# Performance work log

Measured on AMD Instinct MI355X. Metric: run time of the kernel, lower is better.

Reference implementation:

```python
import jax, jax.numpy as jnp
import numpy as np

H, W = 512, 512
B, C = 16, 3
PCT = 3.0  # normalization_percentile_threshold


def _make_filter_map(h, w, d0_ratio=0.05, bn=1):
    d0 = int(max(d0_ratio * min(h, w) // 2, 1))  # = 12 for 512x512
    i = np.arange(h, dtype=np.float64)[:, None]
    j = np.arange(w, dtype=np.float64)[None, :]
    d = np.full((h, w), np.inf)
    for cx, cy in ((0, 0), (0, w - 1), (h - 1, w - 1), (h - 1, 0)):
        d = np.minimum(d, np.sqrt((i - cx) ** 2 + (j - cy) ** 2))
    fm = 1.0 / (1.0 + (d0 / (d + 1.0)) ** (2 * bn))
    # torch code assigns filter_map[j, i] -> transpose (no-op for square sizes)
    return jnp.asarray(fm.T.astype(np.float32))


def setup_inputs() -> dict:
    key = jax.random.key(0)
    k1, k2 = jax.random.split(key)
    x = jax.random.normal(k1, (B, C, H, W), dtype=jnp.float32)
    mask = (jax.random.uniform(k2, (B, C, H, W)) > 0.2).astype(jnp.float32)
    filter_map = _make_filter_map(H, W)
    return {"x": x, "mask": mask, "filter_map": filter_map}


def reference(x, mask, filter_map):
    b, c, h, w = x.shape
    n = h * w
    # median_padding: torch.median returns the lower middle element -> sorted index (n-1)//2
    med = jnp.sort(x.reshape(b, c, n), axis=-1)[..., (n - 1) // 2] + 0.2  # (B,C)
    xp = mask * x + (1.0 - mask) * med[:, :, None, None]
    # Butterworth high-pass in Fourier domain
    hfc = jnp.abs(jnp.fft.ifft2(jnp.fft.fft2(xp) * filter_map)).astype(jnp.float32)
    # per-(n,c) percentile normalization; .int() truncates toward zero -> jnp.trunc
    temp = jnp.trunc(hfc * 256.0) / 256.0
    lo = jnp.percentile(temp, PCT, axis=(-2, -1), keepdims=True)
    hi = jnp.percentile(temp, 100.0 - PCT, axis=(-2, -1), keepdims=True)
    res = (hfc - lo) / (hi - lo)
    return res * mask
```

## Files before the change

kernel.cpp:

```cpp
#include <hip/hip_runtime.h>
#include <math.h>


#define HN 512
#define WN 512
#define NPIX (HN * WN)
#define NCH 48
#define MED_K 131071u
#define TWOPI 6.283185307179586f

typedef unsigned int u32;

__device__ __constant__ u32 PRANKS[4] = {7864u, 7865u, 254278u, 254279u};

__device__ __forceinline__ int rev8_9(int i) { return ((i & 7) << 6) | (i & 56) | (i >> 6); }

#define LPAD 576
__device__ __forceinline__ int padi(int i) { return i + (i >> 3); }

__device__ __forceinline__ u32 f2key(float f) {
  u32 u = __float_as_uint(f);
  return u ^ ((u & 0x80000000u) ? 0xFFFFFFFFu : 0x80000000u);
}
__device__ __forceinline__ float key2f(u32 k) {
  u32 u = (k & 0x80000000u) ? (k ^ 0x80000000u) : ~k;
  return __uint_as_float(u);
}

__device__ __forceinline__ float2 cadd(float2 a, float2 b) { return make_float2(a.x + b.x, a.y + b.y); }
__device__ __forceinline__ float2 csub(float2 a, float2 b) { return make_float2(a.x - b.x, a.y - b.y); }
__device__ __forceinline__ float2 cmul(float2 a, float2 b) {
  return make_float2(a.x * b.x - a.y * b.y, a.x * b.y + a.y * b.x);
}

template <bool INV>
__device__ __forceinline__ void dft8(float2* r) {
  const float S2 = 0.70710678118654752f;
  float2 e0, e1, e2, e3, o0, o1, o2, o3;
  {
    float2 t0 = cadd(r[0], r[4]), t1 = csub(r[0], r[4]);
    float2 t2 = cadd(r[2], r[6]), t3 = csub(r[2], r[6]);
    e0 = cadd(t0, t2); e2 = csub(t0, t2);
    if (!INV) { e1 = make_float2(t1.x + t3.y, t1.y - t3.x); e3 = make_float2(t1.x - t3.y, t1.y + t3.x); }
    else      { e1 = make_float2(t1.x - t3.y, t1.y + t3.x); e3 = make_float2(t1.x + t3.y, t1.y - t3.x); }
  }
  {
    float2 t0 = cadd(r[1], r[5]), t1 = csub(r[1], r[5]);
    float2 t2 = cadd(r[3], r[7]), t3 = csub(r[3], r[7]);
    o0 = cadd(t0, t2); o2 = csub(t0, t2);
    if (!INV) { o1 = make_float2(t1.x + t3.y, t1.y - t3.x); o3 = make_float2(t1.x - t3.y, t1.y + t3.x); }
    else      { o1 = make_float2(t1.x - t3.y, t1.y + t3.x); o3 = make_float2(t1.x + t3.y, t1.y - t3.x); }
  }
  float2 w1o, w2o, w3o;
  if (!INV) {
    w1o = make_float2(S2 * (o1.x + o1.y), S2 * (o1.y - o1.x));
    w2o = make_float2(o2.y, -o2.x);
    w3o = make_float2(S2 * (o3.y - o3.x), -S2 * (o3.x + o3.y));
  } else {
    w1o = make_float2(S2 * (o1.x - o1.y), S2 * (o1.x + o1.y));
    w2o = make_float2(-o2.y, o2.x);
    w3o = make_float2(-S2 * (o3.x + o3.y), S2 * (o3.x - o3.y));
  }
  r[0] = cadd(e0, o0); r[4] = csub(e0, o0);
  r[1] = cadd(e1, w1o); r[5] = csub(e1, w1o);
  r[2] = cadd(e2, w2o); r[6] = csub(e2, w2o);
  r[3] = cadd(e3, w3o); r[7] = csub(e3, w3o);
}

__device__ __forceinline__ void twid(float2* r, float ang) {
  float sn, cs;
  __sincosf(ang, &sn, &cs);
  float2 w = make_float2(cs, sn);
  float2 wj = w;
  r[1] = cmul(r[1], wj);
  #pragma unroll
  for (int j = 2; j < 8; ++j) { wj = cmul(wj, w); r[j] = cmul(r[j], wj); }
}

__device__ void scan_find(const u32* __restrict__ h, int per, u32 rank,
                          u32* out_bin, u32* out_pref) {
  __shared__ u32 csum[256], cpre[256];
  int t = threadIdx.x;
  u32 s = 0;
  for (int i = 0; i < per; ++i) s += h[t * per + i];
  csum[t] = s;
  __syncthreads();
  if (t == 0) { u32 a = 0; for (int i = 0; i < 256; ++i) { cpre[i] = a; a += csum[i]; } }
  __syncthreads();
  if (cpre[t] <= rank && rank < cpre[t] + csum[t]) {
    u32 acc = cpre[t];
    for (int i = 0; i < per; ++i) {
      u32 c = h[t * per + i];
      if (rank < acc + c) { *out_bin = (u32)(t * per + i); *out_pref = acc; break; }
      acc += c;
    }
  }
  __syncthreads();
}


__global__ __launch_bounds__(256) void kmed1(const float4* __restrict__ x4, u32* __restrict__ h1) {
  int ch = blockIdx.x >> 4, s = blockIdx.x & 15;
  __shared__ u32 lh[4096];
  for (int i = threadIdx.x; i < 4096; i += 256) lh[i] = 0;
  __syncthreads();
  const float4* p = x4 + (size_t)ch * (NPIX / 4) + (size_t)s * (NPIX / 64);
  for (int i = threadIdx.x; i < NPIX / 64; i += 256) {
    float4 v = p[i];
    atomicAdd(&lh[f2key(v.x) >> 20], 1u);
    atomicAdd(&lh[f2key(v.y) >> 20], 1u);
    atomicAdd(&lh[f2key(v.z) >> 20], 1u);
    atomicAdd(&lh[f2key(v.w) >> 20], 1u);
  }
  __syncthreads();
  u32* h = h1 + (size_t)ch * 4096;
  for (int i = threadIdx.x; i < 4096; i += 256) { u32 c = lh[i]; if (c) atomicAdd(&h[i], c); }
}

__global__ __launch_bounds__(256) void kscan1(const u32* __restrict__ h1, u32* sel1, u32* pref1) {
  __shared__ u32 b, p;
  scan_find(h1 + (size_t)blockIdx.x * 4096, 16, MED_K, &b, &p);
  if (threadIdx.x == 0) { sel1[blockIdx.x] = b; pref1[blockIdx.x] = p; }
}

__global__ __launch_bounds__(256) void kmed2(const float4* __restrict__ x4, u32* __restrict__ h2,
                                             const u32* __restrict__ sel1) {
  int ch = blockIdx.x >> 4, s = blockIdx.x & 15;
  u32 sh = sel1[ch];
  __shared__ u32 lh[4096];
  for (int i = threadIdx.x; i < 4096; i += 256) lh[i] = 0;
  __syncthreads();
  const float4* p = x4 + (size_t)ch * (NPIX / 4) + (size_t)s * (NPIX / 64);
  for (int i = threadIdx.x; i < NPIX / 64; i += 256) {
    float4 v = p[i];
    u32 k;
    k = f2key(v.x); if ((k >> 20) == sh) atomicAdd(&lh[(k >> 8) & 0xFFFu], 1u);
    k = f2key(v.y); if ((k >> 20) == sh) atomicAdd(&lh[(k >> 8) & 0xFFFu], 1u);
    k = f2key(v.z); if ((k >> 20) == sh) atomicAdd(&lh[(k >> 8) & 0xFFFu], 1u);
    k = f2key(v.w); if ((k >> 20) == sh) atomicAdd(&lh[(k >> 8) & 0xFFFu], 1u);
  }
  __syncthreads();
  u32* h = h2 + (size_t)ch * 4096;
  for (int i = threadIdx.x; i < 4096; i += 256) { u32 c = lh[i]; if (c) atomicAdd(&h[i], c); }
}

__global__ __launch_bounds__(256) void kscan2(const u32* __restrict__ h2, const u32* __restrict__ pref1,
                                              u32* sel2, u32* pref2) {
  __shared__ u32 b, p;
  scan_find(h2 + (size_t)blockIdx.x * 4096, 16, MED_K - pref1[blockIdx.x], &b, &p);
  if (threadIdx.x == 0) { sel2[blockIdx.x] = b; pref2[blockIdx.x] = p; }
}

__global__ __launch_bounds__(256) void kmed3(const float4* __restrict__ x4, u32* __restrict__ h3,
                                             const u32* __restrict__ sel1, const u32* __restrict__ sel2) {
  int ch = blockIdx.x >> 4, s = blockIdx.x & 15;
  u32 pre = (sel1[ch] << 12) | sel2[ch];
  __shared__ u32 lh[256];
  lh[threadIdx.x] = 0;
  __syncthreads();
  const float4* p = x4 + (size_t)ch * (NPIX / 4) + (size_t)s * (NPIX / 64);
  for (int i = threadIdx.x; i < NPIX / 64; i += 256) {
    float4 v = p[i];
    u32 k;
    k = f2key(v.x); if ((k >> 8) == pre) atomicAdd(&lh[k & 0xFFu], 1u);
    k = f2key(v.y); if ((k >> 8) == pre) atomicAdd(&lh[k & 0xFFu], 1u);
    k = f2key(v.z); if ((k >> 8) == pre) atomicAdd(&lh[k & 0xFFu], 1u);
    k = f2key(v.w); if ((k >> 8) == pre) atomicAdd(&lh[k & 0xFFu], 1u);
  }
  __syncthreads();
  u32 c = lh[threadIdx.x];
  if (c) atomicAdd(&h3[(size_t)ch * 256 + threadIdx.x], c);
}

__global__ __launch_bounds__(256) void kscan3(const u32* __restrict__ h3, const u32* __restrict__ sel1,
                                              const u32* __restrict__ sel2, const u32* __restrict__ pref1,
                                              const u32* __restrict__ pref2, float* med) {
  int ch = blockIdx.x;
  __shared__ u32 b, p;
  scan_find(h3 + (size_t)ch * 256, 1, MED_K - pref1[ch] - pref2[ch], &b, &p);
  if (threadIdx.x == 0) {
    u32 key = (sel1[ch] << 20) | (sel2[ch] << 8) | b;
    med[ch] = key2f(key) + 0.2f;
  }
}


__global__ __launch_bounds__(256) void kperm(const float* __restrict__ fmap, float* __restrict__ fmp) {
  int c = blockIdx.x;
  for (int e = threadIdx.x; e < HN; e += 256)
    fmp[(size_t)c * HN + e] = fmap[(size_t)rev8_9(e) * WN + rev8_9(c)] * (1.0f / (float)NPIX);
}


__global__ __launch_bounds__(256) void krow_fwd(const float* __restrict__ x, const float* __restrict__ mask,
                                                const float* __restrict__ med, float2* __restrict__ cbuf, int ch0) {
  int lch = blockIdx.x >> 7, rb = blockIdx.x & 127;
  int gch = ch0 + lch;
  int lane = threadIdx.x & 63, r = threadIdx.x >> 6;
  int row = rb * 4 + r;
  __shared__ float2 lds[4][LPAD];
  float2* L = lds[r];
  float mv = med[gch];
  const float* xr = x + (size_t)gch * NPIX + (size_t)row * WN;
  const float* mr = mask + (size_t)gch * NPIX + (size_t)row * WN;
  float2 rg[8];
  #pragma unroll
  for (int m = 0; m < 8; ++m) {
    float xv = xr[lane + 64 * m], mm = mr[lane + 64 * m];
    rg[m] = make_float2(mm * xv + (1.0f - mm) * mv, 0.0f);
  }
  dft8<false>(rg);
  twid(rg, (float)lane * (-TWOPI / 512.0f));
  int pb = lane + (lane >> 3);
  #pragma unroll
  for (int j = 0; j < 8; ++j) L[pb + 72 * j] = rg[j];
  __syncthreads();
  int n0 = lane & 7;
  int pb2 = 72 * (lane >> 3) + n0;
  #pragma unroll
  for (int m = 0; m < 8; ++m) rg[m] = L[pb2 + 9 * m];
  dft8<false>(rg);
  twid(rg, (float)n0 * (-TWOPI / 64.0f));
  #pragma unroll
  for (int j = 0; j < 8; ++j) L[pb2 + 9 * j] = rg[j];
  __syncthreads();
  int pc = 9 * lane;
  #pragma unroll
  for (int m = 0; m < 8; ++m) rg[m] = L[pc + m];
  dft8<false>(rg);
  #pragma unroll
  for (int j = 0; j < 8; ++j) L[pc + j] = rg[j];
  __syncthreads();
  float2* cb = cbuf + (size_t)lch * NPIX + (size_t)row * WN;
  #pragma unroll
  for (int q = 0; q < 4; ++q) {
    int e = 2 * (lane + 64 * q);
    int pe = padi(e);
    float2 a = L[pe], b = L[pe + 1];
    *(float4*)(cb + e) = make_float4(a.x, a.y, b.x, b.y);
  }
}


__global__ __launch_bounds__(512) void kcol(float2* __restrict__ cbuf, const float* __restrict__ fmp) {
  int lch = blockIdx.x >> 6;
  int c0 = (blockIdx.x & 63) << 3;
  int tid = threadIdx.x;
  int lane = tid & 63, cc = tid >> 6;
  __shared__ float2 lds[8][LPAD];
  float2* L = lds[cc];
  size_t base = (size_t)lch * NPIX + c0;
  #pragma unroll
  for (int it = 0; it < 4; ++it) {
    int g = it * 512 + tid;
    int h = g >> 2, qq = g & 3;
    float4 v = *(const float4*)(cbuf + base + (size_t)h * WN + 2 * qq);
    int ph = padi(h);
    lds[2 * qq][ph]     = make_float2(v.x, v.y);
    lds[2 * qq + 1][ph] = make_float2(v.z, v.w);
  }
  __syncthreads();
  float2 rg[8];
  int pb = lane + (lane >> 3);
  int n0 = lane & 7;
  int pb2 = 72 * (lane >> 3) + n0;
  int pc = 9 * lane;
  #pragma unroll
  for (int m = 0; m < 8; ++m) rg[m] = L[pb + 72 * m];
  dft8<false>(rg);
  twid(rg, (float)lane * (-TWOPI / 512.0f));
  #pragma unroll
  for (int j = 0; j < 8; ++j) L[pb + 72 * j] = rg[j];
  __syncthreads();
  #pragma unroll
  for (int m = 0; m < 8; ++m) rg[m] = L[pb2 + 9 * m];
  dft8<false>(rg);
  twid(rg, (float)n0 * (-TWOPI / 64.0f));
  #pragma unroll
  for (int j = 0; j < 8; ++j) L[pb2 + 9 * j] = rg[j];
  __syncthreads();
  #pragma unroll
  for (int m = 0; m < 8; ++m) rg[m] = L[pc + m];
  dft8<false>(rg);
  {
    const float* fp = fmp + (size_t)(c0 + cc) * HN + 8 * lane;
    float4 f0 = *(const float4*)fp, f1 = *(const float4*)(fp + 4);
    rg[0].x *= f0.x; rg[0].y *= f0.x;  rg[1].x *= f0.y; rg[1].y *= f0.y;
    rg[2].x *= f0.z; rg[2].y *= f0.z;  rg[3].x *= f0.w; rg[3].y *= f0.w;
    rg[4].x *= f1.x; rg[4].y *= f1.x;  rg[5].x *= f1.y; rg[5].y *= f1.y;
    rg[6].x *= f1.z; rg[6].y *= f1.z;  rg[7].x *= f1.w; rg[7].y *= f1.w;
  }
  dft8<true>(rg);
  #pragma unroll
  for (int j = 0; j < 8; ++j) L[pc + j] = rg[j];
  __syncthreads();
  #pragma unroll
  for (int m = 0; m < 8; ++m) rg[m] = L[pb2 + 9 * m];
  twid(rg, (float)n0 * (TWOPI / 64.0f));
  dft8<true>(rg);
  #pragma unroll
  for (int j = 0; j < 8; ++j) L[pb2 + 9 * j] = rg[j];
  __syncthreads();
  #pragma unroll
  for (int m = 0; m < 8; ++m) rg[m] = L[pb + 72 * m];
  twid(rg, (float)lane * (TWOPI / 512.0f));
  dft8<true>(rg);
  #pragma unroll
  for (int j = 0; j < 8; ++j) L[pb + 72 * j] = rg[j];
  __syncthreads();
  #pragma unroll
  for (int it = 0; it < 4; ++it) {
    int g = it * 512 + tid;
    int h = g >> 2, qq = g & 3;
    int ph = padi(h);
    float2 a = lds[2 * qq][ph], b = lds[2 * qq + 1][ph];
    *(float4*)(cbuf + base + (size_t)h * WN + 2 * qq) = make_float4(a.x, a.y, b.x, b.y);
  }
}


__global__ __launch_bounds__(256) void krow_inv(const float2* __restrict__ cbuf, float* __restrict__ out,
                                                u32* __restrict__ hc, int ch0) {
  int lch = blockIdx.x >> 7, rb = blockIdx.x & 127;
  int gch = ch0 + lch;
  int lane = threadIdx.x & 63, r = threadIdx.x >> 6;
  int row = rb * 4 + r;
  __shared__ float2 lds[4][LPAD];
  __shared__ u32 lh[256];
  float2* L = lds[r];
  lh[threadIdx.x] = 0;
  const float2* cb = cbuf + (size_t)lch * NPIX + (size_t)row * WN;
  #pragma unroll
  for (int q = 0; q < 4; ++q) {
    int e = 2 * (lane + 64 * q);
    float4 v = *(const float4*)(cb + e);
    int pe = padi(e);
    L[pe]     = make_float2(v.x, v.y);
    L[pe + 1] = make_float2(v.z, v.w);
  }
  __syncthreads();
  float2 rg[8];
  int pc = 9 * lane;
  #pragma unroll
  for (int m = 0; m < 8; ++m) rg[m] = L[pc + m];
  dft8<true>(rg);
  #pragma unroll
  for (int j = 0; j < 8; ++j) L[pc + j] = rg[j];
  __syncthreads();
  int n0 = lane & 7;
  int pb2 = 72 * (lane >> 3) + n0;
  #pragma unroll
  for (int m = 0; m < 8; ++m) rg[m] = L[pb2 + 9 * m];
  twid(rg, (float)n0 * (TWOPI / 64.0f));
  dft8<true>(rg);
  #pragma unroll
  for (int j = 0; j < 8; ++j) L[pb2 + 9 * j] = rg[j];
  __syncthreads();
  int pb = lane + (lane >> 3);
  #pragma unroll
  for (int m = 0; m < 8; ++m) rg[m] = L[pb + 72 * m];
  twid(rg, (float)lane * (TWOPI / 512.0f));
  dft8<true>(rg);
  float* orow = out + (size_t)gch * NPIX + (size_t)row * WN;
  #pragma unroll
  for (int j = 0; j < 8; ++j) {
    float mg = sqrtf(rg[j].x * rg[j].x + rg[j].y * rg[j].y);
    orow[lane + 64 * j] = mg;
    u32 bin = (u32)fminf(mg * 256.0f, 65535.0f);
    atomicAdd(&lh[bin >> 8], 1u);
  }
  __syncthreads();
  u32 c = lh[threadIdx.x];
  if (c) atomicAdd(&hc[(size_t)gch * 256 + threadIdx.x], c);
}


__global__ __launch_bounds__(256) void kpcts1(const u32* __restrict__ hc, u32* selc, u32* prefc) {
  int ch = blockIdx.x;
  __shared__ u32 b, p;
  for (int q = 0; q < 4; ++q) {
    scan_find(hc + (size_t)ch * 256, 1, PRANKS[q], &b, &p);
    if (threadIdx.x == 0) { selc[ch * 4 + q] = b; prefc[ch * 4 + q] = p; }
    __syncthreads();
  }
}

__global__ __launch_bounds__(256) void kpctf(const float4* __restrict__ out4, u32* __restrict__ hf,
                                             const u32* __restrict__ selc) {
  int ch = blockIdx.x >> 3, s = blockIdx.x & 7;
  u32 t0 = selc[ch * 4 + 0], t1 = selc[ch * 4 + 1], t2 = selc[ch * 4 + 2], t3 = selc[ch * 4 + 3];
  __shared__ u32 lh[1024];
  for (int i = threadIdx.x; i < 1024; i += 256) lh[i] = 0;
  __syncthreads();
  const float4* p = out4 + (size_t)ch * (NPIX / 4) + (size_t)s * (NPIX / 32);
  for (int i = threadIdx.x; i < NPIX / 32; i += 256) {
    float4 v = p[i];
    float vv[4] = {v.x, v.y, v.z, v.w};
    #pragma unroll
    for (int j = 0; j < 4; ++j) {
      u32 bin = (u32)fminf(vv[j] * 256.0f, 65535.0f);
      u32 cb = bin >> 8, fb = bin & 255u;
      if (cb == t0) atomicAdd(&lh[0 * 256 + fb], 1u);
      if (cb == t1) atomicAdd(&lh[1 * 256 + fb], 1u);
      if (cb == t2) atomicAdd(&lh[2 * 256 + fb], 1u);
      if (cb == t3) atomicAdd(&lh[3 * 256 + fb], 1u);
    }
  }
  __syncthreads();
  for (int i = threadIdx.x; i < 1024; i += 256) {
    u32 c = lh[i];
    if (c) atomicAdd(&hf[(size_t)ch * 1024 + i], c);
  }
}

__global__ __launch_bounds__(256) void kpcts2(const u32* __restrict__ hf, const u32* __restrict__ selc,
                                              const u32* __restrict__ prefc, float* lov, float* invv) {
  int ch = blockIdx.x;
  __shared__ u32 b, p;
  __shared__ u32 bins[4];
  for (int q = 0; q < 4; ++q) {
    scan_find(hf + (size_t)ch * 1024 + q * 256, 1, PRANKS[q] - prefc[ch * 4 + q], &b, &p);
    if (threadIdx.x == 0) bins[q] = (selc[ch * 4 + q] << 8) | b;
    __syncthreads();
  }
  if (threadIdx.x == 0) {
    double vlo = 0.03 * (double)(NPIX - 1);
    double vhi = 0.97 * (double)(NPIX - 1);
    double glo = vlo - floor(vlo);
    double ghi = vhi - floor(vhi);
    double l0 = bins[0] / 256.0, l1 = bins[1] / 256.0;
    double h0 = bins[2] / 256.0, h1 = bins[3] / 256.0;
    double lo = l0 + glo * (l1 - l0);
    double hi = h0 + ghi * (h1 - h0);
    lov[ch] = (float)lo;
    invv[ch] = (float)(1.0 / (hi - lo));
  }
}


__global__ __launch_bounds__(256) void kfinal(float4* __restrict__ o4, const float4* __restrict__ m4,
                                              const float* __restrict__ lov, const float* __restrict__ invv) {
  size_t i = (size_t)blockIdx.x * 256 + threadIdx.x;
  int ch = (int)(i >> 16);
  float lo = lov[ch], iv = invv[ch];
  float4 o = o4[i], m = m4[i];
  o.x = (o.x - lo) * iv * m.x;
  o.y = (o.y - lo) * iv * m.y;
  o.z = (o.z - lo) * iv * m.z;
  o.w = (o.w - lo) * iv * m.w;
  o4[i] = o;
}


extern "C" void kernel_launch(void* const* d_in, const int* in_sizes, int n_in,
                              void* d_out, int out_size, void* d_ws, size_t ws_size,
                              hipStream_t stream) {
  (void)in_sizes; (void)n_in; (void)out_size;
  const float* x = (const float*)d_in[0];
  const float* mask = (const float*)d_in[1];
  const float* fmap = (const float*)d_in[2];
  float* out = (float*)d_out;
  char* ws = (char*)d_ws;

  size_t off = 0;
  u32* h1 = (u32*)(ws + off); off += (size_t)NCH * 4096 * 4;
  u32* h2 = (u32*)(ws + off); off += (size_t)NCH * 4096 * 4;
  u32* h3 = (u32*)(ws + off); off += (size_t)NCH * 256 * 4;
  u32* hc = (u32*)(ws + off); off += (size_t)NCH * 256 * 4;
  u32* hf = (u32*)(ws + off); off += (size_t)NCH * 1024 * 4;
  const size_t HIST_BYTES = off;
  u32* sel1  = (u32*)(ws + off); off += NCH * 4;
  u32* pref1 = (u32*)(ws + off); off += NCH * 4;
  u32* sel2  = (u32*)(ws + off); off += NCH * 4;
  u32* pref2 = (u32*)(ws + off); off += NCH * 4;
  u32* selc  = (u32*)(ws + off); off += NCH * 16;
  u32* prefc = (u32*)(ws + off); off += NCH * 16;
  float* med  = (float*)(ws + off); off += NCH * 4;
  float* lov  = (float*)(ws + off); off += NCH * 4;
  float* invv = (float*)(ws + off); off += NCH * 4;
  off = (off + 4095) & ~(size_t)4095;
  float* fmp = (float*)(ws + off); off += (size_t)NPIX * 4;
  off = (off + 255) & ~(size_t)255;
  float2* cbuf = (float2*)(ws + off);

  size_t avail = (ws_size > off) ? ws_size - off : 0;
  int cpc = 1;
  const int cands[8] = {48, 24, 16, 12, 8, 4, 2, 1};
  for (int i = 0; i < 8; ++i) {
    if ((size_t)cands[i] * NPIX * sizeof(float2) <= avail) { cpc = cands[i]; break; }
  }

  hipMemsetAsync(ws, 0, HIST_BYTES, stream);
  kperm<<<WN, 256, 0, stream>>>(fmap, fmp);

  kmed1<<<NCH * 16, 256, 0, stream>>>((const float4*)x, h1);
  kscan1<<<NCH, 256, 0, stream>>>(h1, sel1, pref1);
  kmed2<<<NCH * 16, 256, 0, stream>>>((const float4*)x, h2, sel1);
  kscan2<<<NCH, 256, 0, stream>>>(h2, pref1, sel2, pref2);
  kmed3<<<NCH * 16, 256, 0, stream>>>((const float4*)x, h3, sel1, sel2);
  kscan3<<<NCH, 256, 0, stream>>>(h3, sel1, sel2, pref1, pref2, med);

  for (int ch0 = 0; ch0 < NCH; ch0 += cpc) {
    int cc = (NCH - ch0 < cpc) ? (NCH - ch0) : cpc;
    krow_fwd<<<cc * 128, 256, 0, stream>>>(x, mask, med, cbuf, ch0);
    kcol<<<cc * 64, 512, 0, stream>>>(cbuf, fmp);
    krow_inv<<<cc * 128, 256, 0, stream>>>(cbuf, out, hc, ch0);
  }

  kpcts1<<<NCH, 256, 0, stream>>>(hc, selc, prefc);
  kpctf<<<NCH * 8, 256, 0, stream>>>((const float4*)out, hf, selc);
  kpcts2<<<NCH, 256, 0, stream>>>(hf, selc, prefc, lov, invv);

  kfinal<<<(NCH * NPIX / 4) / 256, 256, 0, stream>>>((float4*)out, (const float4*)mask, lov, invv);
}
```

Baseline: 372.2 us.

## Swizzle LDS FFT layout, use wave barriers, widen column tiles, aggregate histogram atomics

Replaces the padded shared-memory layout with an XOR swizzle. Because each wave now owns its own row or column buffer, the block-wide __syncthreads between FFT stages become wave barriers. The column kernel handles 16 columns per 1024-thread block instead of 8. The inverse-row histogram moves to per-wave bins, and ballot-based aggregation collapses equal bins into one atomic. The final normalization uses nontemporal stores. The aim is to cut bank conflicts, barrier cost and atomic contention, at the cost of larger blocks, more LDS per block and serial ballot loops.

```diff
diff --git a/kernel.cpp b/kernel.cpp
--- a/kernel.cpp
+++ b/kernel.cpp
@@ -10,13 +10,15 @@
 #define TWOPI 6.283185307179586f
 
 typedef unsigned int u32;
+typedef float f4v __attribute__((ext_vector_type(4)));
 
 __device__ __constant__ u32 PRANKS[4] = {7864u, 7865u, 254278u, 254279u};
 
 __device__ __forceinline__ int rev8_9(int i) { return ((i & 7) << 6) | (i & 56) | (i >> 6); }
 
-#define LPAD 576
-__device__ __forceinline__ int padi(int i) { return i + (i >> 3); }
+__device__ __forceinline__ int swz(int e) { return e ^ ((e >> 4) & 0xF); }
+
+#define WB() __builtin_amdgcn_wave_barrier()
 
 __device__ __forceinline__ u32 f2key(float f) {
   u32 u = __float_as_uint(f);
@@ -198,7 +200,7 @@
   int gch = ch0 + lch;
   int lane = threadIdx.x & 63, r = threadIdx.x >> 6;
   int row = rb * 4 + r;
-  __shared__ float2 lds[4][LPAD];
+  __shared__ float2 lds[4][512];
   float2* L = lds[r];
   float mv = med[gch];
   const float* xr = x + (size_t)gch * NPIX + (size_t)row * WN;
@@ -211,79 +213,75 @@
   }
   dft8<false>(rg);
   twid(rg, (float)lane * (-TWOPI / 512.0f));
-  int pb = lane + (lane >> 3);
-  #pragma unroll
-  for (int j = 0; j < 8; ++j) L[pb + 72 * j] = rg[j];
-  __syncthreads();
-  int n0 = lane & 7;
-  int pb2 = 72 * (lane >> 3) + n0;
-  #pragma unroll
-  for (int m = 0; m < 8; ++m) rg[m] = L[pb2 + 9 * m];
+  #pragma unroll
+  for (int j = 0; j < 8; ++j) L[swz(lane + 64 * j)] = rg[j];
+  WB();
+  int eb = 64 * (lane >> 3) + (lane & 7);
+  #pragma unroll
+  for (int m = 0; m < 8; ++m) rg[m] = L[swz(eb + 8 * m)];
   dft8<false>(rg);
-  twid(rg, (float)n0 * (-TWOPI / 64.0f));
-  #pragma unroll
-  for (int j = 0; j < 8; ++j) L[pb2 + 9 * j] = rg[j];
-  __syncthreads();
-  int pc = 9 * lane;
-  #pragma unroll
-  for (int m = 0; m < 8; ++m) rg[m] = L[pc + m];
+  twid(rg, (float)(lane & 7) * (-TWOPI / 64.0f));
+  #pragma unroll
+  for (int j = 0; j < 8; ++j) L[swz(eb + 8 * j)] = rg[j];
+  WB();
+  int pcb = (8 * lane) ^ ((lane >> 1) & 0xF);
+  #pragma unroll
+  for (int m = 0; m < 8; ++m) rg[m] = L[pcb ^ m];
   dft8<false>(rg);
   #pragma unroll
-  for (int j = 0; j < 8; ++j) L[pc + j] = rg[j];
-  __syncthreads();
+  for (int j = 0; j < 8; ++j) L[pcb ^ j] = rg[j];
+  WB();
   float2* cb = cbuf + (size_t)lch * NPIX + (size_t)row * WN;
   #pragma unroll
   for (int q = 0; q < 4; ++q) {
     int e = 2 * (lane + 64 * q);
-    int pe = padi(e);
-    float2 a = L[pe], b = L[pe + 1];
+    int s = swz(e);
+    float2 a = L[s], b = L[s ^ 1];
     *(float4*)(cb + e) = make_float4(a.x, a.y, b.x, b.y);
   }
 }
 
 
-__global__ __launch_bounds__(512) void kcol(float2* __restrict__ cbuf, const float* __restrict__ fmp) {
-  int lch = blockIdx.x >> 6;
-  int c0 = (blockIdx.x & 63) << 3;
+__global__ __launch_bounds__(1024, 8) void kcol(float2* __restrict__ cbuf, const float* __restrict__ fmp) {
+  int lch = blockIdx.x >> 5;
+  int c0 = (blockIdx.x & 31) << 4;
   int tid = threadIdx.x;
-  int lane = tid & 63, cc = tid >> 6;
-  __shared__ float2 lds[8][LPAD];
-  float2* L = lds[cc];
+  int lane = tid & 63, w = tid >> 6;
+  __shared__ float2 lds[16][512];
+  float2* L = lds[w];
   size_t base = (size_t)lch * NPIX + c0;
   #pragma unroll
   for (int it = 0; it < 4; ++it) {
-    int g = it * 512 + tid;
-    int h = g >> 2, qq = g & 3;
+    int g = it * 1024 + tid;
+    int h = g >> 3, qq = g & 7;
     float4 v = *(const float4*)(cbuf + base + (size_t)h * WN + 2 * qq);
-    int ph = padi(h);
-    lds[2 * qq][ph]     = make_float2(v.x, v.y);
-    lds[2 * qq + 1][ph] = make_float2(v.z, v.w);
+    int sh = swz(h);
+    lds[2 * qq][sh]     = make_float2(v.x, v.y);
+    lds[2 * qq + 1][sh] = make_float2(v.z, v.w);
   }
   __syncthreads();
   float2 rg[8];
-  int pb = lane + (lane >> 3);
-  int n0 = lane & 7;
-  int pb2 = 72 * (lane >> 3) + n0;
-  int pc = 9 * lane;
-  #pragma unroll
-  for (int m = 0; m < 8; ++m) rg[m] = L[pb + 72 * m];
+  int eb = 64 * (lane >> 3) + (lane & 7);
+  int pcb = (8 * lane) ^ ((lane >> 1) & 0xF);
+  #pragma unroll
+  for (int m = 0; m < 8; ++m) rg[m] = L[swz(lane + 64 * m)];
   dft8<false>(rg);
   twid(rg, (float)lane * (-TWOPI / 512.0f));
   #pragma unroll
-  for (int j = 0; j < 8; ++j) L[pb + 72 * j] = rg[j];
-  __syncthreads();
-  #pragma unroll
-  for (int m = 0; m < 8; ++m) rg[m] = L[pb2 + 9 * m];
+  for (int j = 0; j < 8; ++j) L[swz(lane + 64 * j)] = rg[j];
+  WB();
+  #pragma unroll
+  for (int m = 0; m < 8; ++m) rg[m] = L[swz(eb + 8 * m)];
   dft8<false>(rg);
-  twid(rg, (float)n0 * (-TWOPI / 64.0f));
-  #pragma unroll
-  for (int j = 0; j < 8; ++j) L[pb2 + 9 * j] = rg[j];
-  __syncthreads();
-  #pragma unroll
-  for (int m = 0; m < 8; ++m) rg[m] = L[pc + m];
+  twid(rg, (float)(lane & 7) * (-TWOPI / 64.0f));
+  #pragma unroll
+  for (int j = 0; j < 8; ++j) L[swz(eb + 8 * j)] = rg[j];
+  WB();
+  #pragma unroll
+  for (int m = 0; m < 8; ++m) rg[m] = L[pcb ^ m];
   dft8<false>(rg);
   {
-    const float* fp = fmp + (size_t)(c0 + cc) * HN + 8 * lane;
+    const float* fp = fmp + (size_t)(c0 + w) * HN + 8 * lane;
     float4 f0 = *(const float4*)fp, f1 = *(const float4*)(fp + 4);
     rg[0].x *= f0.x; rg[0].y *= f0.x;  rg[1].x *= f0.y; rg[1].y *= f0.y;
     rg[2].x *= f0.z; rg[2].y *= f0.z;  rg[3].x *= f0.w; rg[3].y *= f0.w;
@@ -292,28 +290,28 @@
   }
   dft8<true>(rg);
   #pragma unroll
-  for (int j = 0; j < 8; ++j) L[pc + j] = rg[j];
-  __syncthreads();
-  #pragma unroll
-  for (int m = 0; m < 8; ++m) rg[m] = L[pb2 + 9 * m];
-  twid(rg, (float)n0 * (TWOPI / 64.0f));
+  for (int j = 0; j < 8; ++j) L[pcb ^ j] = rg[j];
+  WB();
+  #pragma unroll
+  for (int m = 0; m < 8; ++m) rg[m] = L[swz(eb + 8 * m)];
+  twid(rg, (float)(lane & 7) * (TWOPI / 64.0f));
   dft8<true>(rg);
   #pragma unroll
-  for (int j = 0; j < 8; ++j) L[pb2 + 9 * j] = rg[j];
-  __syncthreads();
-  #pragma unroll
-  for (int m = 0; m < 8; ++m) rg[m] = L[pb + 72 * m];
+  for (int j = 0; j < 8; ++j) L[swz(eb + 8 * j)] = rg[j];
+  WB();
+  #pragma unroll
+  for (int m = 0; m < 8; ++m) rg[m] = L[swz(lane + 64 * m)];
   twid(rg, (float)lane * (TWOPI / 512.0f));
   dft8<true>(rg);
   #pragma unroll
-  for (int j = 0; j < 8; ++j) L[pb + 72 * j] = rg[j];
+  for (int j = 0; j < 8; ++j) L[swz(lane + 64 * j)] = rg[j];
   __syncthreads();
   #pragma unroll
   for (int it = 0; it < 4; ++it) {
-    int g = it * 512 + tid;
-    int h = g >> 2, qq = g & 3;
-    int ph = padi(h);
-    float2 a = lds[2 * qq][ph], b = lds[2 * qq + 1][ph];
+    int g = it * 1024 + tid;
+    int h = g >> 3, qq = g & 7;
+    int sh = swz(h);
+    float2 a = lds[2 * qq][sh], b = lds[2 * qq + 1][sh];
     *(float4*)(cbuf + base + (size_t)h * WN + 2 * qq) = make_float4(a.x, a.y, b.x, b.y);
   }
 }
@@ -325,53 +323,67 @@
   int gch = ch0 + lch;
   int lane = threadIdx.x & 63, r = threadIdx.x >> 6;
   int row = rb * 4 + r;
-  __shared__ float2 lds[4][LPAD];
-  __shared__ u32 lh[256];
+  __shared__ float2 lds[4][512];
+  __shared__ u32 lh[4][256];
   float2* L = lds[r];
-  lh[threadIdx.x] = 0;
+  u32* H = lh[r];
+  #pragma unroll
+  for (int i = 0; i < 4; ++i) H[lane + 64 * i] = 0;
   const float2* cb = cbuf + (size_t)lch * NPIX + (size_t)row * WN;
   #pragma unroll
   for (int q = 0; q < 4; ++q) {
     int e = 2 * (lane + 64 * q);
     float4 v = *(const float4*)(cb + e);
-    int pe = padi(e);
-    L[pe]     = make_float2(v.x, v.y);
-    L[pe + 1] = make_float2(v.z, v.w);
-  }
-  __syncthreads();
+    int s = swz(e);
+    L[s]     = make_float2(v.x, v.y);
+    L[s ^ 1] = make_float2(v.z, v.w);
+  }
+  WB();
   float2 rg[8];
-  int pc = 9 * lane;
-  #pragma unroll
-  for (int m = 0; m < 8; ++m) rg[m] = L[pc + m];
+  int pcb = (8 * lane) ^ ((lane >> 1) & 0xF);
+  #pragma unroll
+  for (int m = 0; m < 8; ++m) rg[m] = L[pcb ^ m];
   dft8<true>(rg);
   #pragma unroll
-  for (int j = 0; j < 8; ++j) L[pc + j] = rg[j];
-  __syncthreads();
-  int n0 = lane & 7;
-  int pb2 = 72 * (lane >> 3) + n0;
-  #pragma unroll
-  for (int m = 0; m < 8; ++m) rg[m] = L[pb2 + 9 * m];
-  twid(rg, (float)n0 * (TWOPI / 64.0f));
+  for (int j = 0; j < 8; ++j) L[pcb ^ j] = rg[j];
+  WB();
+  int eb = 64 * (lane >> 3) + (lane & 7);
+  #pragma unroll
+  for (int m = 0; m < 8; ++m) rg[m] = L[swz(eb + 8 * m)];
+  twid(rg, (float)(lane & 7) * (TWOPI / 64.0f));
   dft8<true>(rg);
   #pragma unroll
-  for (int j = 0; j < 8; ++j) L[pb2 + 9 * j] = rg[j];
-  __syncthreads();
-  int pb = lane + (lane >> 3);
-  #pragma unroll
-  for (int m = 0; m < 8; ++m) rg[m] = L[pb + 72 * m];
+  for (int j = 0; j < 8; ++j) L[swz(eb + 8 * j)] = rg[j];
+  WB();
+  #pragma unroll
+  for (int m = 0; m < 8; ++m) rg[m] = L[swz(lane + 64 * m)];
   twid(rg, (float)lane * (TWOPI / 512.0f));
   dft8<true>(rg);
   float* orow = out + (size_t)gch * NPIX + (size_t)row * WN;
+  u32 binv[8];
   #pragma unroll
   for (int j = 0; j < 8; ++j) {
     float mg = sqrtf(rg[j].x * rg[j].x + rg[j].y * rg[j].y);
     orow[lane + 64 * j] = mg;
-    u32 bin = (u32)fminf(mg * 256.0f, 65535.0f);
-    atomicAdd(&lh[bin >> 8], 1u);
-  }
-  __syncthreads();
-  u32 c = lh[threadIdx.x];
-  if (c) atomicAdd(&hc[(size_t)gch * 256 + threadIdx.x], c);
+    binv[j] = ((u32)fminf(mg * 256.0f, 65535.0f)) >> 8;
+  }
+  #pragma unroll 1
+  for (int j = 0; j < 8; ++j) {
+    u32 bin = binv[j];
+    unsigned long long todo = __ballot(1);
+    while (todo) {
+      int src = (int)(__ffsll((unsigned long long)todo) - 1);
+      u32 b = (u32)__shfl((int)bin, src);
+      unsigned long long mt = __ballot(bin == b);
+      if (lane == src) atomicAdd(&H[b], (u32)__popcll(mt));
+      todo &= ~mt;
+    }
+  }
+  #pragma unroll
+  for (int i = 0; i < 4; ++i) {
+    u32 c = H[lane + 64 * i];
+    if (c) atomicAdd(&hc[(size_t)gch * 256 + lane + 64 * i], c);
+  }
 }
 
 
@@ -444,11 +456,12 @@
   int ch = (int)(i >> 16);
   float lo = lov[ch], iv = invv[ch];
   float4 o = o4[i], m = m4[i];
-  o.x = (o.x - lo) * iv * m.x;
-  o.y = (o.y - lo) * iv * m.y;
-  o.z = (o.z - lo) * iv * m.z;
-  o.w = (o.w - lo) * iv * m.w;
-  o4[i] = o;
+  f4v res;
+  res.x = (o.x - lo) * iv * m.x;
+  res.y = (o.y - lo) * iv * m.y;
+  res.z = (o.z - lo) * iv * m.z;
+  res.w = (o.w - lo) * iv * m.w;
+  __builtin_nontemporal_store(res, (f4v*)&o4[i]);
 }
 
 
@@ -490,7 +503,7 @@
     if ((size_t)cands[i] * NPIX * sizeof(float2) <= avail) { cpc = cands[i]; break; }
   }
 
-  hipMemsetAsync(ws, 0, HIST_BYTES, stream);
+  (void)hipMemsetAsync(ws, 0, HIST_BYTES, stream);
   kperm<<<WN, 256, 0, stream>>>(fmap, fmp);
 
   kmed1<<<NCH * 16, 256, 0, stream>>>((const float4*)x, h1);
@@ -503,7 +516,7 @@
   for (int ch0 = 0; ch0 < NCH; ch0 += cpc) {
     int cc = (NCH - ch0 < cpc) ? (NCH - ch0) : cpc;
     krow_fwd<<<cc * 128, 256, 0, stream>>>(x, mask, med, cbuf, ch0);
-    kcol<<<cc * 64, 512, 0, stream>>>(cbuf, fmp);
+    kcol<<<cc * 32, 1024, 0, stream>>>(cbuf, fmp);
     krow_inv<<<cc * 128, 256, 0, stream>>>(cbuf, out, hc, ch0);
   }
 
```

New measurement: 366.8 us. No clear change (-1.5%).
